# Performance work log

Hardware: AMD Instinct MI355X
Metric: run time of the kernel (lower is better)

## Reference

```python
import jax, jax.numpy as jnp
import numpy as np

NUM_HEADS = 8
D_MODEL = 512
D_Q = D_MODEL // NUM_HEADS
B, S = 4, 2048


def setup_inputs() -> dict:
    key = jax.random.key(0)
    ks = jax.random.split(key, 7)
    bound = 1.0 / np.sqrt(D_MODEL)  # kaiming_uniform with a=sqrt(5) on fan_in=d_model
    return {
        "x_query": jax.random.normal(ks[0], (B, S, D_MODEL), dtype=jnp.float32),
        "x_key": jax.random.normal(ks[1], (B, S, D_MODEL), dtype=jnp.float32),
        "x_value": jax.random.normal(ks[2], (B, S, D_MODEL), dtype=jnp.float32),
        "Q": jax.random.uniform(ks[3], (NUM_HEADS, D_MODEL, D_Q), minval=-bound, maxval=bound, dtype=jnp.float32),
        "K": jax.random.uniform(ks[4], (NUM_HEADS, D_MODEL, D_Q), minval=-bound, maxval=bound, dtype=jnp.float32),
        "V": jax.random.uniform(ks[5], (NUM_HEADS, D_MODEL, D_Q), minval=-bound, maxval=bound, dtype=jnp.float32),
        "Wout": jax.random.uniform(ks[6], (D_MODEL, D_MODEL), minval=-bound, maxval=bound, dtype=jnp.float32),
    }


def reference(x_query, x_key, x_value, Q, K, V, Wout):
    # per-head projections: [B,S,d_model] x [H,d_model,d_q] -> [B,H,S,d_q]
    q = jnp.einsum('bsd,hdq->bhsq', x_query, Q)
    k = jnp.einsum('bsd,hdq->bhsq', x_key, K)
    v = jnp.einsum('bsd,hdq->bhsq', x_value, V)
    scale = 1.0 / jnp.sqrt(jnp.asarray(q.shape[-1], q.dtype))
    scores = jnp.einsum('bhsq,bhtq->bhst', q, k) * scale  # [B,H,S,S]
    attn = jax.nn.softmax(scores, axis=-1)
    heads = jnp.einsum('bhst,bhtq->bhsq', attn, v)  # [B,H,S,d_q]
    # faithful to original: .view(B, S, -1) on [B,H,S,d_q] layout (no transpose)
    concat = heads.reshape(heads.shape[0], heads.shape[2], -1)
    return concat @ Wout.T
```

## Files before the change

kernel.cpp:

```cpp
#include <hip/hip_runtime.h>
#include <math.h>

#define BATCH 4
#define SEQ   2048
#define DM    512
#define NH    8
#define DQ    64
#define BS    (BATCH*SEQ)
#define BPAD  72
#define APAD  72

#define QSCALE 0.18033688011112042f

typedef short  short8  __attribute__((ext_vector_type(8)));
typedef float  floatx4 __attribute__((ext_vector_type(4)));
typedef unsigned short ushort8 __attribute__((ext_vector_type(8)));

__device__ __forceinline__ unsigned short f2bf(float f) {
    return (unsigned short)((__float_as_uint(f) + 0x8000u) >> 16);
}
__device__ __forceinline__ unsigned pack2bf(float a, float b) {
    unsigned ua = __float_as_uint(a) + 0x8000u;
    unsigned ub = __float_as_uint(b) + 0x8000u;
    return __builtin_amdgcn_perm(ub, ua, 0x07060302u);
}

__device__ __forceinline__ void async_copy16(const void* g, void* l) {
    __builtin_amdgcn_global_load_lds(
        (const __attribute__((address_space(1))) unsigned int*)g,
        (__attribute__((address_space(3))) unsigned int*)l, 16, 0, 0);
}

__global__ __launch_bounds__(256) void convert_w_kernel(
    const float* __restrict__ Wq, const float* __restrict__ Wk,
    const float* __restrict__ Wv, const float* __restrict__ Wo,
    unsigned short* __restrict__ wt, unsigned short* __restrict__ wo)
{
    const int which = blockIdx.y;
    const int idx = blockIdx.x * 256 + threadIdx.x;
    if (which == 3) {
        float4 v = *(const float4*)(Wo + (size_t)idx * 4);
        uint2 o;
        o.x = pack2bf(v.x, v.y);
        o.y = pack2bf(v.z, v.w);
        *(uint2*)(wo + (size_t)idx * 4) = o;
    } else {
        const float* W = (which == 0) ? Wq : (which == 1) ? Wk : Wv;
        const int n   = idx >> 7;
        const int dd0 = (idx & 127) * 4;
        const int h = n >> 6, d = n & 63;
        uint2 o;
        o.x = pack2bf(W[((size_t)h * DM + dd0 + 0) * DQ + d],
                      W[((size_t)h * DM + dd0 + 1) * DQ + d]);
        o.y = pack2bf(W[((size_t)h * DM + dd0 + 2) * DQ + d],
                      W[((size_t)h * DM + dd0 + 3) * DQ + d]);
        *(uint2*)(wt + (size_t)which * (DM * DM) + (size_t)n * DM + dd0) = o;
    }
}

__global__ __launch_bounds__(256) void qkv_gemm_kernel(
    const float* __restrict__ Xq, const float* __restrict__ Xk,
    const float* __restrict__ Xv, const unsigned short* __restrict__ wt,
    unsigned short* __restrict__ Oq, unsigned short* __restrict__ Ok,
    unsigned short* __restrict__ Ovt)
{
    __shared__ unsigned short As[128][APAD];
    __shared__ unsigned short Bs[128][64];

    const int which = blockIdx.z;
    const float* X = (which == 0) ? Xq : (which == 1) ? Xk : Xv;
    const unsigned short* Bt = wt + (size_t)which * (DM * DM);

    const int m0 = blockIdx.x * 128;
    const int n0 = blockIdx.y * 128;
    const int t = threadIdx.x, w = t >> 6, lane = t & 63;
    const int quad = lane >> 4, qr = lane & 15;
    const int lr = lane >> 3;
    const int lc = (lane & 7) * 8;
    const int arow = t >> 4;
    const int acol = (t & 15) * 4;
    const int mw = 64 * (w >> 1), nw = 64 * (w & 1);

    floatx4 acc[4][4] = {};

    for (int k0 = 0; k0 < DM; k0 += 64) {
        #pragma unroll
        for (int i = 0; i < 4; ++i) {
            const int row = i * 32 + w * 8;
            async_copy16(Bt + (size_t)(n0 + row + lr) * DM + k0 + lc, &Bs[row][0]);
        }
        #pragma unroll
        for (int i = 0; i < 8; ++i) {
            const int row = i * 16 + arow;
            float4 x4 = *(const float4*)(X + (size_t)(m0 + row) * DM + k0 + acol);
            uint2 o;
            o.x = pack2bf(x4.x, x4.y);
            o.y = pack2bf(x4.z, x4.w);
            *(uint2*)&As[row][acol] = o;
        }
        __syncthreads();
        #pragma unroll
        for (int kh = 0; kh < 2; ++kh) {
            short8 af[4], bf[4];
            #pragma unroll
            for (int si = 0; si < 4; ++si)
                af[si] = *(const short8*)&As[mw + 16 * si + qr][kh * 32 + quad * 8];
            #pragma unroll
            for (int sj = 0; sj < 4; ++sj)
                bf[sj] = *(const short8*)&Bs[nw + 16 * sj + qr][kh * 32 + quad * 8];
            #pragma unroll
            for (int si = 0; si < 4; ++si)
                #pragma unroll
                for (int sj = 0; sj < 4; ++sj)
                    acc[si][sj] = __builtin_amdgcn_mfma_f32_16x16x32_bf16(
                        af[si], bf[sj], acc[si][sj], 0, 0, 0);
        }
        __syncthreads();
    }

    const float osc = (which == 0) ? QSCALE : 1.0f;
    if (which < 2) {
        unsigned short* O = (which == 0) ? Oq : Ok;
        #pragma unroll
        for (int si = 0; si < 4; ++si) {
            #pragma unroll
            for (int sj = 0; sj < 4; ++sj) {
                const int col = n0 + nw + 16 * sj + qr;
                const int h = col >> 6, d = col & 63;
                #pragma unroll
                for (int r = 0; r < 4; ++r) {
                    const int row = m0 + mw + 16 * si + quad * 4 + r;
                    const int b = row >> 11, s = row & (SEQ - 1);
                    O[((size_t)(b * NH + h) * SEQ + s) * DQ + d] = f2bf(acc[si][sj][r] * osc);
                }
            }
        }
    } else {
        #pragma unroll
        for (int si = 0; si < 4; ++si) {
            #pragma unroll
            for (int sj = 0; sj < 4; ++sj) {
                const int col = n0 + nw + 16 * sj + qr;
                const int h = col >> 6, d = col & 63;
                #pragma unroll
                for (int r = 0; r < 4; ++r) {
                    const int row = m0 + mw + 16 * si + quad * 4 + r;
                    const int b = row >> 11, s = row & (SEQ - 1);
                    Ovt[((size_t)(b * NH + h) * DQ + d) * SEQ + s] = f2bf(acc[si][sj][r]);
                }
            }
        }
    }
}

__global__ __launch_bounds__(256) void out_gemm_kernel(
    const unsigned short* __restrict__ A, const unsigned short* __restrict__ Bt,
    float* __restrict__ C)
{
    __shared__ unsigned short As[128][64];
    __shared__ unsigned short Bs[128][64];

    const int m0 = blockIdx.x * 128;
    const int n0 = blockIdx.y * 128;
    const int t = threadIdx.x, w = t >> 6, lane = t & 63;
    const int quad = lane >> 4, qr = lane & 15;
    const int lr = lane >> 3;
    const int lc = (lane & 7) * 8;
    const int mw = 64 * (w >> 1), nw = 64 * (w & 1);

    floatx4 acc[4][4] = {};

    for (int k0 = 0; k0 < DM; k0 += 64) {
        #pragma unroll
        for (int i = 0; i < 4; ++i) {
            const int row = i * 32 + w * 8;
            async_copy16(A  + (size_t)(m0 + row + lr) * DM + k0 + lc, &As[row][0]);
            async_copy16(Bt + (size_t)(n0 + row + lr) * DM + k0 + lc, &Bs[row][0]);
        }
        __syncthreads();
        #pragma unroll
        for (int kh = 0; kh < 2; ++kh) {
            short8 af[4], bf[4];
            #pragma unroll
            for (int si = 0; si < 4; ++si)
                af[si] = *(const short8*)&As[mw + 16 * si + qr][kh * 32 + quad * 8];
            #pragma unroll
            for (int sj = 0; sj < 4; ++sj)
                bf[sj] = *(const short8*)&Bs[nw + 16 * sj + qr][kh * 32 + quad * 8];
            #pragma unroll
            for (int si = 0; si < 4; ++si)
                #pragma unroll
                for (int sj = 0; sj < 4; ++sj)
                    acc[si][sj] = __builtin_amdgcn_mfma_f32_16x16x32_bf16(
                        af[si], bf[sj], acc[si][sj], 0, 0, 0);
        }
        __syncthreads();
    }

    #pragma unroll
    for (int si = 0; si < 4; ++si) {
        #pragma unroll
        for (int sj = 0; sj < 4; ++sj) {
            const int col = n0 + nw + 16 * sj + qr;
            #pragma unroll
            for (int r = 0; r < 4; ++r) {
                const int row = m0 + mw + 16 * si + quad * 4 + r;
                C[(size_t)row * DM + col] = acc[si][sj][r];
            }
        }
    }
}

__global__ __launch_bounds__(256) void attn_kernel(
    const unsigned short* __restrict__ Qp, const unsigned short* __restrict__ Kp,
    const unsigned short* __restrict__ Vtp, unsigned short* __restrict__ Hd)
{
    __shared__ unsigned short Qs[64][BPAD];
    __shared__ unsigned short Ks[64][BPAD];
    __shared__ unsigned short Vts[64][BPAD];
    __shared__ unsigned short Ps[64][BPAD];

    const int s0 = blockIdx.x * 64;
    const int h  = blockIdx.y;
    const int b  = blockIdx.z;
    const size_t bh    = (size_t)(b * NH + h);
    const size_t base  = bh * SEQ * DQ;
    const size_t vbase = bh * DQ * SEQ;

    const int t    = threadIdx.x;
    const int w    = t >> 6;
    const int lane = t & 63;
    const int quad = lane >> 4;
    const int qr   = lane & 15;

    {
        const unsigned short* g = Qp + base + (size_t)s0 * DQ;
        #pragma unroll
        for (int i = 0; i < 2; ++i) {
            const int c = t + 256 * i;
            const int row = c >> 3, col8 = (c & 7) * 8;
            *(ushort8*)&Qs[row][col8] = *(const ushort8*)(g + row * DQ + col8);
        }
    }
    __syncthreads();
    const short8 aq0 = *(const short8*)&Qs[16 * w + qr][quad * 8];
    const short8 aq1 = *(const short8*)&Qs[16 * w + qr][quad * 8 + 32];

    floatx4 acc_o[4] = {};
    float l_lane = 0.f;

    ushort8 kreg[2], vreg[2];
    {
        const unsigned short* gk = Kp + base;
        const unsigned short* gv = Vtp + vbase;
        #pragma unroll
        for (int i = 0; i < 2; ++i) {
            const int c = t + 256 * i;
            const int row = c >> 3, col8 = (c & 7) * 8;
            kreg[i] = *(const ushort8*)(gk + row * DQ + col8);
            vreg[i] = *(const ushort8*)(gv + (size_t)row * SEQ + col8);
        }
    }

    for (int kt = 0; kt < SEQ; kt += 64) {
        __syncthreads();
        #pragma unroll
        for (int i = 0; i < 2; ++i) {
            const int c = t + 256 * i;
            const int row = c >> 3, col8 = (c & 7) * 8;
            *(ushort8*)&Ks[row][col8]  = kreg[i];
            *(ushort8*)&Vts[row][col8] = vreg[i];
        }
        __syncthreads();

        if (kt + 64 < SEQ) {
            const unsigned short* gk = Kp + base + (size_t)(kt + 64) * DQ;
            const unsigned short* gv = Vtp + vbase + (kt + 64);
            #pragma unroll
            for (int i = 0; i < 2; ++i) {
                const int c = t + 256 * i;
                const int row = c >> 3, col8 = (c & 7) * 8;
                kreg[i] = *(const ushort8*)(gk + row * DQ + col8);
                vreg[i] = *(const ushort8*)(gv + (size_t)row * SEQ + col8);
            }
        }

        #pragma unroll
        for (int si = 0; si < 4; ++si) {
            const short8 ak0 = *(const short8*)&Ks[16 * si + qr][quad * 8];
            const short8 ak1 = *(const short8*)&Ks[16 * si + qr][quad * 8 + 32];
            floatx4 z = {0.f, 0.f, 0.f, 0.f};
            z = __builtin_amdgcn_mfma_f32_16x16x32_bf16(ak0, aq0, z, 0, 0, 0);
            z = __builtin_amdgcn_mfma_f32_16x16x32_bf16(ak1, aq1, z, 0, 0, 0);
            const float p0 = exp2f(z[0]), p1 = exp2f(z[1]);
            const float p2 = exp2f(z[2]), p3 = exp2f(z[3]);
            l_lane += (p0 + p1) + (p2 + p3);
            uint2 pk;
            pk.x = pack2bf(p0, p1);
            pk.y = pack2bf(p2, p3);
            *(uint2*)&Ps[16 * w + qr][16 * si + quad * 4] = pk;
        }

        const short8 ap0 = *(const short8*)&Ps[16 * w + qr][quad * 8];
        const short8 ap1 = *(const short8*)&Ps[16 * w + qr][quad * 8 + 32];
        #pragma unroll
        for (int c = 0; c < 4; ++c) {
            const short8 bv0 = *(const short8*)&Vts[16 * c + qr][quad * 8];
            const short8 bv1 = *(const short8*)&Vts[16 * c + qr][quad * 8 + 32];
            acc_o[c] = __builtin_amdgcn_mfma_f32_16x16x32_bf16(ap0, bv0, acc_o[c], 0, 0, 0);
            acc_o[c] = __builtin_amdgcn_mfma_f32_16x16x32_bf16(ap1, bv1, acc_o[c], 0, 0, 0);
        }
    }

    l_lane += __shfl_xor(l_lane, 16);
    l_lane += __shfl_xor(l_lane, 32);
    float inv_l[4];
    #pragma unroll
    for (int r = 0; r < 4; ++r)
        inv_l[r] = 1.0f / __shfl(l_lane, quad * 4 + r);

    #pragma unroll
    for (int c = 0; c < 4; ++c)
        #pragma unroll
        for (int r = 0; r < 4; ++r)
            Hd[base + (size_t)(s0 + 16 * w + quad * 4 + r) * DQ + 16 * c + qr] =
                f2bf(acc_o[c][r] * inv_l[r]);
}

extern "C" void kernel_launch(void* const* d_in, const int* in_sizes, int n_in,
                              void* d_out, int out_size, void* d_ws, size_t ws_size,
                              hipStream_t stream) {
    const float* xq = (const float*)d_in[0];
    const float* xk = (const float*)d_in[1];
    const float* xv = (const float*)d_in[2];
    const float* Qw = (const float*)d_in[3];
    const float* Kw = (const float*)d_in[4];
    const float* Vw = (const float*)d_in[5];
    const float* Wo = (const float*)d_in[6];
    float* out = (float*)d_out;

    unsigned short* ws = (unsigned short*)d_ws;
    unsigned short* wt    = ws;
    unsigned short* wo    = ws + (size_t)786432;
    unsigned short* q_ws  = ws + (size_t)1048576;
    unsigned short* k_ws  = ws + (size_t)5242880;
    unsigned short* vt_ws = ws + (size_t)9437184;
    unsigned short* h_ws  = ws + (size_t)13631488;

    convert_w_kernel<<<dim3(256, 4), 256, 0, stream>>>(Qw, Kw, Vw, Wo, wt, wo);
    qkv_gemm_kernel<<<dim3(64, 4, 3), 256, 0, stream>>>(xq, xk, xv, wt, q_ws, k_ws, vt_ws);
    attn_kernel<<<dim3(SEQ / 64, NH, BATCH), 256, 0, stream>>>(q_ws, k_ws, vt_ws, h_ws);
    out_gemm_kernel<<<dim3(64, 4), 256, 0, stream>>>(h_ws, wo, out);
}
```

Before: 215.2 us.

## Register-prefetch GEMM tiles, halve out-GEMM M tile, use native exp2

```diff
diff --git a/kernel.cpp b/kernel.cpp
--- a/kernel.cpp
+++ b/kernel.cpp
@@ -23,12 +23,6 @@
     unsigned ua = __float_as_uint(a) + 0x8000u;
     unsigned ub = __float_as_uint(b) + 0x8000u;
     return __builtin_amdgcn_perm(ub, ua, 0x07060302u);
-}
-
-__device__ __forceinline__ void async_copy16(const void* g, void* l) {
-    __builtin_amdgcn_global_load_lds(
-        (const __attribute__((address_space(1))) unsigned int*)g,
-        (__attribute__((address_space(3))) unsigned int*)l, 16, 0, 0);
 }
 
 __global__ __launch_bounds__(256) void convert_w_kernel(
@@ -65,7 +59,7 @@
     unsigned short* __restrict__ Ovt)
 {
     __shared__ unsigned short As[128][APAD];
-    __shared__ unsigned short Bs[128][64];
+    __shared__ unsigned short Bs[128][APAD];
 
     const int which = blockIdx.z;
     const float* X = (which == 0) ? Xq : (which == 1) ? Xk : Xv;
@@ -75,30 +69,46 @@
     const int n0 = blockIdx.y * 128;
     const int t = threadIdx.x, w = t >> 6, lane = t & 63;
     const int quad = lane >> 4, qr = lane & 15;
-    const int lr = lane >> 3;
-    const int lc = (lane & 7) * 8;
     const int arow = t >> 4;
     const int acol = (t & 15) * 4;
+    const int brow = t >> 3;
+    const int bcol = (t & 7) * 8;
     const int mw = 64 * (w >> 1), nw = 64 * (w & 1);
 
     floatx4 acc[4][4] = {};
+    float4  areg[8];
+    ushort8 breg[4];
+
+    #pragma unroll
+    for (int i = 0; i < 8; ++i)
+        areg[i] = *(const float4*)(X + (size_t)(m0 + i * 16 + arow) * DM + acol);
+    #pragma unroll
+    for (int i = 0; i < 4; ++i)
+        breg[i] = *(const ushort8*)(Bt + (size_t)(n0 + i * 32 + brow) * DM + bcol);
 
     for (int k0 = 0; k0 < DM; k0 += 64) {
-        #pragma unroll
-        for (int i = 0; i < 4; ++i) {
-            const int row = i * 32 + w * 8;
-            async_copy16(Bt + (size_t)(n0 + row + lr) * DM + k0 + lc, &Bs[row][0]);
-        }
+        __syncthreads();
         #pragma unroll
         for (int i = 0; i < 8; ++i) {
-            const int row = i * 16 + arow;
-            float4 x4 = *(const float4*)(X + (size_t)(m0 + row) * DM + k0 + acol);
             uint2 o;
-            o.x = pack2bf(x4.x, x4.y);
-            o.y = pack2bf(x4.z, x4.w);
-            *(uint2*)&As[row][acol] = o;
-        }
-        __syncthreads();
+            o.x = pack2bf(areg[i].x, areg[i].y);
+            o.y = pack2bf(areg[i].z, areg[i].w);
+            *(uint2*)&As[i * 16 + arow][acol] = o;
+        }
+        #pragma unroll
+        for (int i = 0; i < 4; ++i)
+            *(ushort8*)&Bs[i * 32 + brow][bcol] = breg[i];
+        __syncthreads();
+
+        if (k0 + 64 < DM) {
+            #pragma unroll
+            for (int i = 0; i < 8; ++i)
+                areg[i] = *(const float4*)(X + (size_t)(m0 + i * 16 + arow) * DM + k0 + 64 + acol);
+            #pragma unroll
+            for (int i = 0; i < 4; ++i)
+                breg[i] = *(const ushort8*)(Bt + (size_t)(n0 + i * 32 + brow) * DM + k0 + 64 + bcol);
+        }
+
         #pragma unroll
         for (int kh = 0; kh < 2; ++kh) {
             short8 af[4], bf[4];
@@ -115,7 +125,6 @@
                     acc[si][sj] = __builtin_amdgcn_mfma_f32_16x16x32_bf16(
                         af[si], bf[sj], acc[si][sj], 0, 0, 0);
         }
-        __syncthreads();
     }
 
     const float osc = (which == 0) ? QSCALE : 1.0f;
@@ -157,48 +166,66 @@
     const unsigned short* __restrict__ A, const unsigned short* __restrict__ Bt,
     float* __restrict__ C)
 {
-    __shared__ unsigned short As[128][64];
-    __shared__ unsigned short Bs[128][64];
-
-    const int m0 = blockIdx.x * 128;
+    __shared__ unsigned short As[64][APAD];
+    __shared__ unsigned short Bs[128][APAD];
+
+    const int m0 = blockIdx.x * 64;
     const int n0 = blockIdx.y * 128;
     const int t = threadIdx.x, w = t >> 6, lane = t & 63;
     const int quad = lane >> 4, qr = lane & 15;
-    const int lr = lane >> 3;
-    const int lc = (lane & 7) * 8;
-    const int mw = 64 * (w >> 1), nw = 64 * (w & 1);
-
-    floatx4 acc[4][4] = {};
+    const int brow = t >> 3;
+    const int bcol = (t & 7) * 8;
+    const int mw = 32 * (w >> 1), nw = 64 * (w & 1);
+
+    floatx4 acc[2][4] = {};
+    ushort8 areg[2], breg[4];
+
+    #pragma unroll
+    for (int i = 0; i < 2; ++i)
+        areg[i] = *(const ushort8*)(A + (size_t)(m0 + i * 32 + brow) * DM + bcol);
+    #pragma unroll
+    for (int i = 0; i < 4; ++i)
+        breg[i] = *(const ushort8*)(Bt + (size_t)(n0 + i * 32 + brow) * DM + bcol);
 
     for (int k0 = 0; k0 < DM; k0 += 64) {
-        #pragma unroll
-        for (int i = 0; i < 4; ++i) {
-            const int row = i * 32 + w * 8;
-            async_copy16(A  + (size_t)(m0 + row + lr) * DM + k0 + lc, &As[row][0]);
-            async_copy16(Bt + (size_t)(n0 + row + lr) * DM + k0 + lc, &Bs[row][0]);
-        }
-        __syncthreads();
+        __syncthreads();
+        #pragma unroll
+        for (int i = 0; i < 2; ++i)
+            *(ushort8*)&As[i * 32 + brow][bcol] = areg[i];
+        #pragma unroll
+        for (int i = 0; i < 4; ++i)
+            *(ushort8*)&Bs[i * 32 + brow][bcol] = breg[i];
+        __syncthreads();
+
+        if (k0 + 64 < DM) {
+            #pragma unroll
+            for (int i = 0; i < 2; ++i)
+                areg[i] = *(const ushort8*)(A + (size_t)(m0 + i * 32 + brow) * DM + k0 + 64 + bcol);
+            #pragma unroll
+            for (int i = 0; i < 4; ++i)
+                breg[i] = *(const ushort8*)(Bt + (size_t)(n0 + i * 32 + brow) * DM + k0 + 64 + bcol);
+        }
+
         #pragma unroll
         for (int kh = 0; kh < 2; ++kh) {
-            short8 af[4], bf[4];
-            #pragma unroll
-            for (int si = 0; si < 4; ++si)
+            short8 af[2], bf[4];
+            #pragma unroll
+            for (int si = 0; si < 2; ++si)
                 af[si] = *(const short8*)&As[mw + 16 * si + qr][kh * 32 + quad * 8];
             #pragma unroll
             for (int sj = 0; sj < 4; ++sj)
                 bf[sj] = *(const short8*)&Bs[nw + 16 * sj + qr][kh * 32 + quad * 8];
             #pragma unroll
-            for (int si = 0; si < 4; ++si)
+            for (int si = 0; si < 2; ++si)
                 #pragma unroll
                 for (int sj = 0; sj < 4; ++sj)
                     acc[si][sj] = __builtin_amdgcn_mfma_f32_16x16x32_bf16(
                         af[si], bf[sj], acc[si][sj], 0, 0, 0);
         }
-        __syncthreads();
-    }
-
-    #pragma unroll
-    for (int si = 0; si < 4; ++si) {
+    }
+
+    #pragma unroll
+    for (int si = 0; si < 2; ++si) {
         #pragma unroll
         for (int sj = 0; sj < 4; ++sj) {
             const int col = n0 + nw + 16 * sj + qr;
@@ -292,8 +319,10 @@
             floatx4 z = {0.f, 0.f, 0.f, 0.f};
             z = __builtin_amdgcn_mfma_f32_16x16x32_bf16(ak0, aq0, z, 0, 0, 0);
             z = __builtin_amdgcn_mfma_f32_16x16x32_bf16(ak1, aq1, z, 0, 0, 0);
-            const float p0 = exp2f(z[0]), p1 = exp2f(z[1]);
-            const float p2 = exp2f(z[2]), p3 = exp2f(z[3]);
+            const float p0 = __builtin_amdgcn_exp2f(z[0]);
+            const float p1 = __builtin_amdgcn_exp2f(z[1]);
+            const float p2 = __builtin_amdgcn_exp2f(z[2]);
+            const float p3 = __builtin_amdgcn_exp2f(z[3]);
             l_lane += (p0 + p1) + (p2 + p3);
             uint2 pk;
             pk.x = pack2bf(p0, p1);
@@ -350,5 +379,5 @@
     convert_w_kernel<<<dim3(256, 4), 256, 0, stream>>>(Qw, Kw, Vw, Wo, wt, wo);
     qkv_gemm_kernel<<<dim3(64, 4, 3), 256, 0, stream>>>(xq, xk, xv, wt, q_ws, k_ws, vt_ws);
     attn_kernel<<<dim3(SEQ / 64, NH, BATCH), 256, 0, stream>>>(q_ws, k_ws, vt_ws, h_ws);
-    out_gemm_kernel<<<dim3(64, 4), 256, 0, stream>>>(h_ws, wo, out);
-}
+    out_gemm_kernel<<<dim3(128, 4), 256, 0, stream>>>(h_ws, wo, out);
+}
```

Result: faster. 197.0 us (-8.5%).
